# Optimization experiments

Measured on AMD Instinct MI355X. Metric: run time of the kernel, lower is better.

Reference implementation:

```python
import jax, jax.numpy as jnp
import numpy as np

N_NODES = 50000
N_EDGES = 600000
N_GRAPHS = 64
D = 128  # node/edge/global feature dim
NUM_CLASSES = 10
NUM_PASSES = 3


def setup_inputs() -> dict:
    key = jax.random.key(0)
    ks = jax.random.split(key, 12)
    node_attr = jax.random.normal(ks[0], (N_NODES, D), jnp.float32)
    edge_attr = jax.random.normal(ks[1], (N_EDGES, D), jnp.float32)
    u = jax.random.normal(ks[2], (N_GRAPHS, D), jnp.float32)
    edge_index = jax.random.randint(ks[3], (2, N_EDGES), 0, N_NODES, jnp.int64 if jax.config.jax_enable_x64 else jnp.int32)
    batch = jnp.sort(jax.random.randint(ks[4], (N_NODES,), 0, N_GRAPHS, jnp.int32))
    s = 1.0 / np.sqrt(D)
    We_w = jax.random.normal(ks[5], (4 * D, D), jnp.float32) * s
    We_b = jnp.zeros((D,), jnp.float32)
    Wn_w = jax.random.normal(ks[6], (3 * D, D), jnp.float32) * s
    Wn_b = jnp.zeros((D,), jnp.float32)
    Wg_w = jax.random.normal(ks[7], (3 * D, D), jnp.float32) * s
    Wg_b = jnp.zeros((D,), jnp.float32)
    lin_w = jax.random.normal(ks[8], (3 * D, NUM_CLASSES), jnp.float32) * s
    lin_b = jnp.zeros((NUM_CLASSES,), jnp.float32)
    return {"node_attr": node_attr, "edge_attr": edge_attr, "u": u,
            "edge_index": edge_index, "batch": batch,
            "We_w": We_w, "We_b": We_b, "Wn_w": Wn_w, "Wn_b": Wn_b,
            "Wg_w": Wg_w, "Wg_b": Wg_b, "lin_w": lin_w, "lin_b": lin_b}


def _segment_mean(x, seg, num_segments):
    s = jax.ops.segment_sum(x, seg, num_segments=num_segments)
    cnt = jax.ops.segment_sum(jnp.ones((x.shape[0],), x.dtype), seg, num_segments=num_segments)
    return s / jnp.maximum(cnt, 1.0)[:, None]


def reference(node_attr, edge_attr, u, edge_index, batch,
              We_w, We_b, Wn_w, Wn_b, Wg_w, Wg_b, lin_w, lin_b):
    src = edge_index[0]
    dst = edge_index[1]
    n_nodes = node_attr.shape[0]
    n_graphs = u.shape[0]
    edge_bar = None
    for _ in range(NUM_PASSES):
        # edge update: phi_e([h_src, h_dst, e, u[batch_src]])
        e_in = jnp.concatenate(
            [node_attr[src], node_attr[dst], edge_attr, u[batch[src]]], axis=1)
        edge_attr = jax.nn.relu(e_in @ We_w + We_b)
        # node update: mean of incoming edges per dest node, then phi_n
        edge_bar = _segment_mean(edge_attr, dst, n_nodes)  # [N, D]
        n_in = jnp.concatenate([node_attr, edge_bar, u[batch]], axis=1)
        node_attr = jax.nn.relu(n_in @ Wn_w + Wn_b)
        # global update: per-graph means, then phi_g
        node_mean = _segment_mean(node_attr, batch, n_graphs)
        eb_mean = _segment_mean(edge_bar, batch, n_graphs)
        g_in = jnp.concatenate([node_mean, eb_mean, u], axis=1)
        u = jax.nn.relu(g_in @ Wg_w + Wg_b)
    # readout: concat + global mean pool + linear classifier
    graph_attr = jnp.concatenate([node_attr, edge_bar, u[batch]], axis=1)  # [N, 3D]
    pooled = _segment_mean(graph_attr, batch, n_graphs)  # [G, 3D]
    return pooled @ lin_w + lin_b
```

## Files before the change

kernel.cpp:

```cpp
#include <hip/hip_runtime.h>
#include <math.h>

#define D 128

typedef short bf16x8 __attribute__((ext_vector_type(8)));
typedef float f32x4 __attribute__((ext_vector_type(4)));

__device__ __forceinline__ ushort f2b(float f) {
    union { float f; unsigned u; } v; v.f = f;
    unsigned r = v.u + 0x7FFFu + ((v.u >> 16) & 1u);
    return (ushort)(r >> 16);
}
__device__ __forceinline__ float b2f(ushort b) {
    union { unsigned u; float f; } v; v.u = ((unsigned)b) << 16;
    return v.f;
}
__device__ __forceinline__ void gl_lds16(const void* g, void* l) {
    __builtin_amdgcn_global_load_lds(
        (const __attribute__((address_space(1))) void*)g,
        (__attribute__((address_space(3))) void*)l, 16, 0, 0);
}
__device__ __forceinline__ int lower_bound_i(const int* __restrict__ a, int n, int v) {
    int lo = 0, hi = n;
    while (lo < hi) { int m = (lo + hi) >> 1; if (a[m] < v) lo = m + 1; else hi = m; }
    return lo;
}

__global__ void count_kernel(const int* __restrict__ dst, int* __restrict__ cnt, int E) {
    int e = blockIdx.x * blockDim.x + threadIdx.x;
    if (e < E) atomicAdd(&cnt[dst[e]], 1);
}

__global__ void scan_kernel(const int* __restrict__ cnt, int* __restrict__ offs, int N) {
    __shared__ int part[1024];
    const int t = threadIdx.x;
    const int chunk = (N + 1023) >> 10;
    int lo = t * chunk; if (lo > N) lo = N;
    int hi = lo + chunk; if (hi > N) hi = N;
    int s = 0;
    for (int i = lo; i < hi; ++i) s += cnt[i];
    part[t] = s;
    __syncthreads();
    if (t == 0) {
        int a = 0;
        for (int i = 0; i < 1024; ++i) { int v = part[i]; part[i] = a; a += v; }
        offs[N] = a;
    }
    __syncthreads();
    int a = part[t];
    for (int i = lo; i < hi; ++i) { offs[i] = a; a += cnt[i]; }
}

__global__ void scatter_kernel(const int* __restrict__ dst, const int* __restrict__ offs,
                               int* __restrict__ fill, int* __restrict__ csr, int E) {
    int e = blockIdx.x * blockDim.x + threadIdx.x;
    if (e < E) {
        int d = dst[e];
        int p = offs[d] + atomicAdd(&fill[d], 1);
        csr[p] = e;
    }
}

__global__ void f2b_kernel(const float* __restrict__ in, ushort* __restrict__ out, int n) {
    int i = blockIdx.x * blockDim.x + threadIdx.x;
    if (i < n) out[i] = f2b(in[i]);
}

__global__ void conv_edge_kernel(float* __restrict__ edge, int E) {
    int gid = blockIdx.x * blockDim.x + threadIdx.x;
    if (gid < E * 32) {
        int row = gid >> 5, q = gid & 31;
        float4 v = *(const float4*)(edge + (size_t)row * D + q * 4);
        ushort4 o;
        o.x = f2b(v.x); o.y = f2b(v.y); o.z = f2b(v.z); o.w = f2b(v.w);
        *(ushort4*)((ushort*)edge + (size_t)row * 256 + q * 4) = o;
    }
}

__global__ void transpose_w(const float* __restrict__ W, ushort* __restrict__ Wt, int K) {
    int i = blockIdx.x * blockDim.x + threadIdx.x;
    if (i < K * D) { int k = i >> 7, n = i & 127; Wt[(size_t)n * K + k] = f2b(W[i]); }
}

__global__ __launch_bounds__(256) void edge_gemm(
    const ushort* __restrict__ node_bf, ushort* __restrict__ edge_u,
    const ushort* __restrict__ u_bf,
    const int* __restrict__ src, const int* __restrict__ dst,
    const int* __restrict__ batch,
    const ushort* __restrict__ Wt, const float* __restrict__ bias, int E)
{
    __shared__ ushort As[128 * 32];
    __shared__ ushort Bs[128 * 32];
    __shared__ int rs[128], rd[128], rb[128];

    const int tid = threadIdx.x;
    const int w = tid >> 6, l = tid & 63;
    const int e0 = blockIdx.x * 128;

    if (tid < 128) {
        int e = e0 + tid; if (e >= E) e = E - 1;
        int s = src[e];
        rs[tid] = s; rd[tid] = dst[e]; rb[tid] = batch[s];
    }

    f32x4 acc[4][4];
#pragma unroll
    for (int i = 0; i < 4; ++i)
#pragma unroll
        for (int j = 0; j < 4; ++j) acc[i][j] = (f32x4)0.0f;

    const int wm = (w >> 1) * 64, wn = (w & 1) * 64;
    float bj4[4];
#pragma unroll
    for (int j = 0; j < 4; ++j) bj4[j] = bias[wn + j * 16 + (l & 15)];

    const int srow = l >> 2;
    const int part = (l & 3) * 8;

    __syncthreads();

    for (int c = 0; c < 16; ++c) {
        const int srcsel = c >> 2;
        const int kl = (c & 3) * 32;

#pragma unroll
        for (int t = 0; t < 2; ++t) {
            const int s = w + t * 4;
            const int row = s * 16 + srow;
            const ushort* gp;
            if (srcsel == 0)      gp = node_bf + (size_t)rs[row] * D + kl + part;
            else if (srcsel == 1) gp = node_bf + (size_t)rd[row] * D + kl + part;
            else if (srcsel == 2) { int e = e0 + row; if (e >= E) e = E - 1;
                                    gp = edge_u + (size_t)e * 256 + kl + part; }
            else                  gp = u_bf + (size_t)rb[row] * D + kl + part;
            gl_lds16(gp, &As[s * 512]);
        }
#pragma unroll
        for (int t = 0; t < 2; ++t) {
            const int s = w + t * 4;
            const int n = s * 16 + srow;
            gl_lds16(Wt + (size_t)n * 512 + c * 32 + part, &Bs[s * 512]);
        }
        __syncthreads();

        bf16x8 af[4], bfr[4];
#pragma unroll
        for (int i = 0; i < 4; ++i)
            af[i] = *(const bf16x8*)&As[(wm + i * 16 + (l & 15)) * 32 + (l >> 4) * 8];
#pragma unroll
        for (int j = 0; j < 4; ++j)
            bfr[j] = *(const bf16x8*)&Bs[(wn + j * 16 + (l & 15)) * 32 + (l >> 4) * 8];
#pragma unroll
        for (int i = 0; i < 4; ++i)
#pragma unroll
            for (int j = 0; j < 4; ++j)
                acc[i][j] = __builtin_amdgcn_mfma_f32_16x16x32_bf16(af[i], bfr[j], acc[i][j], 0, 0, 0);
        __syncthreads();
    }

#pragma unroll
    for (int i = 0; i < 4; ++i) {
#pragma unroll
        for (int r = 0; r < 4; ++r) {
            const int m = wm + i * 16 + (l >> 4) * 4 + r;
            const int e = e0 + m;
            if (e < E) {
                ushort* ep = edge_u + (size_t)e * 256;
#pragma unroll
                for (int j = 0; j < 4; ++j) {
                    float v = fmaxf(acc[i][j][r] + bj4[j], 0.0f);
                    ep[wn + j * 16 + (l & 15)] = f2b(v);
                }
            }
        }
    }
}

__global__ void gather_ebar(const ushort* __restrict__ edge_u, const int* __restrict__ offs,
                            const int* __restrict__ csr, ushort* __restrict__ ebar_bf, int N)
{
    int n = blockIdx.x * 2 + (threadIdx.x >> 7);
    int col = threadIdx.x & 127;
    if (n >= N) return;
    int lo = offs[n], hi = offs[n + 1];
    float s = 0.0f;
    for (int j = lo; j < hi; ++j) {
        int e = csr[j];
        s += b2f(edge_u[(size_t)e * 256 + col]);
    }
    ebar_bf[(size_t)n * D + col] = f2b(s / (float)max(hi - lo, 1));
}

__global__ __launch_bounds__(256) void node_gemm(
    ushort* __restrict__ node_bf, const ushort* __restrict__ ebar_bf,
    const ushort* __restrict__ u_bf, const int* __restrict__ batch,
    const ushort* __restrict__ Wt, const float* __restrict__ bias, int N)
{
    __shared__ ushort As[128 * 32];
    __shared__ ushort Bs[128 * 32];
    __shared__ int rb[128];

    const int tid = threadIdx.x;
    const int w = tid >> 6, l = tid & 63;
    const int n0 = blockIdx.x * 128;

    if (tid < 128) {
        int n = n0 + tid; if (n >= N) n = N - 1;
        rb[tid] = batch[n];
    }

    f32x4 acc[4][4];
#pragma unroll
    for (int i = 0; i < 4; ++i)
#pragma unroll
        for (int j = 0; j < 4; ++j) acc[i][j] = (f32x4)0.0f;

    const int wm = (w >> 1) * 64, wn = (w & 1) * 64;
    float bj4[4];
#pragma unroll
    for (int j = 0; j < 4; ++j) bj4[j] = bias[wn + j * 16 + (l & 15)];

    const int srow = l >> 2;
    const int part = (l & 3) * 8;

    __syncthreads();

    for (int c = 0; c < 12; ++c) {
        const int srcsel = c >> 2;
        const int kl = (c & 3) * 32;

#pragma unroll
        for (int t = 0; t < 2; ++t) {
            const int s = w + t * 4;
            const int row = s * 16 + srow;
            int n = n0 + row; if (n >= N) n = N - 1;
            const ushort* gp;
            if (srcsel == 0)      gp = node_bf + (size_t)n * D + kl + part;
            else if (srcsel == 1) gp = ebar_bf + (size_t)n * D + kl + part;
            else                  gp = u_bf + (size_t)rb[row] * D + kl + part;
            gl_lds16(gp, &As[s * 512]);
        }
#pragma unroll
        for (int t = 0; t < 2; ++t) {
            const int s = w + t * 4;
            const int n = s * 16 + srow;
            gl_lds16(Wt + (size_t)n * 384 + c * 32 + part, &Bs[s * 512]);
        }
        __syncthreads();

        bf16x8 af[4], bfr[4];
#pragma unroll
        for (int i = 0; i < 4; ++i)
            af[i] = *(const bf16x8*)&As[(wm + i * 16 + (l & 15)) * 32 + (l >> 4) * 8];
#pragma unroll
        for (int j = 0; j < 4; ++j)
            bfr[j] = *(const bf16x8*)&Bs[(wn + j * 16 + (l & 15)) * 32 + (l >> 4) * 8];
#pragma unroll
        for (int i = 0; i < 4; ++i)
#pragma unroll
            for (int j = 0; j < 4; ++j)
                acc[i][j] = __builtin_amdgcn_mfma_f32_16x16x32_bf16(af[i], bfr[j], acc[i][j], 0, 0, 0);
        __syncthreads();
    }

#pragma unroll
    for (int i = 0; i < 4; ++i) {
#pragma unroll
        for (int r = 0; r < 4; ++r) {
            const int m = wm + i * 16 + (l >> 4) * 4 + r;
            const int n = n0 + m;
            if (n < N) {
#pragma unroll
                for (int j = 0; j < 4; ++j) {
                    float v = fmaxf(acc[i][j][r] + bj4[j], 0.0f);
                    node_bf[(size_t)n * D + wn + j * 16 + (l & 15)] = f2b(v);
                }
            }
        }
    }
}

__global__ void reduce_partial(
    const ushort* __restrict__ node_bf, const ushort* __restrict__ ebar_bf,
    const int* __restrict__ batch,
    float* __restrict__ nsum, float* __restrict__ esum, int N)
{
    const int col = threadIdx.x & 127;
    const int half = threadIdx.x >> 7;
    const int r0 = blockIdx.x * 128;
    float sn = 0.0f, se = 0.0f;
    int cur = -1;
    for (int ri = half; ri < 128; ri += 2) {
        int r = r0 + ri;
        if (r >= N) break;
        int g = batch[r];
        if (g != cur) {
            if (cur >= 0) {
                atomicAdd(&nsum[cur * D + col], sn);
                atomicAdd(&esum[cur * D + col], se);
            }
            cur = g; sn = 0.0f; se = 0.0f;
        }
        sn += b2f(node_bf[(size_t)r * D + col]);
        se += b2f(ebar_bf[(size_t)r * D + col]);
    }
    if (cur >= 0) {
        atomicAdd(&nsum[cur * D + col], sn);
        atomicAdd(&esum[cur * D + col], se);
    }
}

__global__ void finalize_means(
    const float* __restrict__ nsum, const float* __restrict__ esum,
    const int* __restrict__ batch,
    float* __restrict__ nmean, float* __restrict__ emean, int N)
{
    const int g = blockIdx.x;
    const int j = threadIdx.x;
    __shared__ int cnt_s;
    if (j == 0) {
        int lo = lower_bound_i(batch, N, g);
        int hi = lower_bound_i(batch, N, g + 1);
        cnt_s = hi - lo;
    }
    __syncthreads();
    float inv = 1.0f / (float)max(cnt_s, 1);
    nmean[g * D + j] = nsum[g * D + j] * inv;
    emean[g * D + j] = esum[g * D + j] * inv;
}

__global__ void global_kernel(
    const float* __restrict__ nmean, const float* __restrict__ emean,
    float* __restrict__ u, ushort* __restrict__ u_bf,
    const float* __restrict__ W, const float* __restrict__ bias)
{
    __shared__ float gin[384];
    const int g = blockIdx.x;
    const int j = threadIdx.x;
    gin[j]       = nmean[g * D + j];
    gin[128 + j] = emean[g * D + j];
    gin[256 + j] = u[g * D + j];
    __syncthreads();
    float s = bias[j];
    for (int k = 0; k < 384; ++k) s += gin[k] * W[(size_t)k * D + j];
    float v = fmaxf(s, 0.0f);
    u[g * D + j] = v;
    u_bf[g * D + j] = f2b(v);
}

__global__ void out_kernel(
    const float* __restrict__ nmean, const float* __restrict__ emean,
    const float* __restrict__ u, const int* __restrict__ batch,
    const float* __restrict__ lw, const float* __restrict__ lb,
    float* __restrict__ out, int N, int NC)
{
    __shared__ float pin[384];
    __shared__ int cntg;
    const int g = blockIdx.x;
    const int t = threadIdx.x;
    if (t == 0) {
        int lo = lower_bound_i(batch, N, g);
        int hi = lower_bound_i(batch, N, g + 1);
        cntg = hi - lo;
    }
    __syncthreads();
    if (t < 128)       pin[t] = nmean[g * D + t];
    else if (t < 256)  pin[t] = emean[g * D + (t - 128)];
    else               pin[t] = (cntg > 0) ? u[g * D + (t - 256)] : 0.0f;
    __syncthreads();
    int c = t >> 5, wv = t & 31;
    if (c < NC) {
        float s = 0.0f;
        for (int k = wv; k < 384; k += 32) s += pin[k] * lw[(size_t)k * NC + c];
#pragma unroll
        for (int off = 16; off > 0; off >>= 1) s += __shfl_down(s, off, 32);
        if (wv == 0) out[g * NC + c] = s + lb[c];
    }
}

extern "C" void kernel_launch(void* const* d_in, const int* in_sizes, int n_in,
                              void* d_out, int out_size, void* d_ws, size_t ws_size,
                              hipStream_t stream) {
    float* node = (float*)d_in[0];
    float* edge = (float*)d_in[1];
    float* u    = (float*)d_in[2];
    const int* eidx  = (const int*)d_in[3];
    const int* batch = (const int*)d_in[4];
    const float* We_w = (const float*)d_in[5];
    const float* We_b = (const float*)d_in[6];
    const float* Wn_w = (const float*)d_in[7];
    const float* Wn_b = (const float*)d_in[8];
    const float* Wg_w = (const float*)d_in[9];
    const float* Wg_b = (const float*)d_in[10];
    const float* lin_w = (const float*)d_in[11];
    const float* lin_b = (const float*)d_in[12];

    const int N = in_sizes[0] / D;
    const int E = in_sizes[3] / 2;
    const int G = in_sizes[2] / D;
    const int NC = out_size / G;
    const int* src = eidx;
    const int* dst = eidx + E;

    char* p = (char*)d_ws;
    auto carve = [&](size_t bytes) { void* r = p; p += (bytes + 255) & ~(size_t)255; return r; };
    ushort* node_bf = (ushort*)carve((size_t)N * D * 2);
    ushort* ebar_bf = (ushort*)carve((size_t)N * D * 2);
    ushort* u_bf    = (ushort*)carve((size_t)G * D * 2);
    ushort* Wet     = (ushort*)carve((size_t)512 * D * 2);
    ushort* Wnt     = (ushort*)carve((size_t)384 * D * 2);
    int*    cnt     = (int*)carve((size_t)N * 4);
    int*    offs    = (int*)carve((size_t)(N + 1) * 4);
    int*    fill    = (int*)carve((size_t)N * 4);
    int*    csr     = (int*)carve((size_t)E * 4);
    float*  nmean   = (float*)carve((size_t)G * D * 4);
    float*  emean   = (float*)carve((size_t)G * D * 4);
    float*  nsum    = (float*)carve((size_t)G * D * 4);
    float*  esum    = (float*)carve((size_t)G * D * 4);

    ushort* edge_u = (ushort*)edge;

    hipMemsetAsync(cnt, 0, (size_t)N * 4, stream);
    hipMemsetAsync(fill, 0, (size_t)N * 4, stream);
    count_kernel<<<(E + 255) / 256, 256, 0, stream>>>(dst, cnt, E);
    scan_kernel<<<1, 1024, 0, stream>>>(cnt, offs, N);
    scatter_kernel<<<(E + 255) / 256, 256, 0, stream>>>(dst, offs, fill, csr, E);

    f2b_kernel<<<(N * D + 255) / 256, 256, 0, stream>>>(node, node_bf, N * D);
    f2b_kernel<<<(G * D + 255) / 256, 256, 0, stream>>>(u, u_bf, G * D);
    transpose_w<<<(512 * D + 255) / 256, 256, 0, stream>>>(We_w, Wet, 512);
    transpose_w<<<(384 * D + 255) / 256, 256, 0, stream>>>(Wn_w, Wnt, 384);
    conv_edge_kernel<<<(E * 32 + 255) / 256, 256, 0, stream>>>(edge, E);

    const int edge_blocks = (E + 127) / 128;
    const int node_blocks = (N + 127) / 128;
    const int red_blocks  = (N + 127) / 128;

    for (int pass = 0; pass < 3; ++pass) {
        edge_gemm<<<edge_blocks, 256, 0, stream>>>(node_bf, edge_u, u_bf, src, dst, batch,
                                                   Wet, We_b, E);
        gather_ebar<<<(N + 1) / 2, 256, 0, stream>>>(edge_u, offs, csr, ebar_bf, N);
        node_gemm<<<node_blocks, 256, 0, stream>>>(node_bf, ebar_bf, u_bf, batch,
                                                   Wnt, Wn_b, N);
        hipMemsetAsync(nsum, 0, (size_t)G * D * 4, stream);
        hipMemsetAsync(esum, 0, (size_t)G * D * 4, stream);
        reduce_partial<<<red_blocks, 256, 0, stream>>>(node_bf, ebar_bf, batch, nsum, esum, N);
        finalize_means<<<G, 128, 0, stream>>>(nsum, esum, batch, nmean, emean, N);
        global_kernel<<<G, 128, 0, stream>>>(nmean, emean, u, u_bf, Wg_w, Wg_b);
    }
    out_kernel<<<G, 384, 0, stream>>>(nmean, emean, u, batch, lin_w, lin_b,
                                      (float*)d_out, N, NC);
}
```

Before: 1.505 ms.

## Fuse prep kernels, enlarge edge GEMM tile, vectorize gather, merge global update

The five conversion and transpose kernels become one prep kernel, and finalize_means is merged with global_kernel. The merged kernel zeroes the sums itself, so the per-pass memsets go away and the setup memsets become one. The edge GEMM tile grows to 256 rows by the full 128 columns per block, with each wave doing 64x128. This halves the weight loads per row and the block count, but doubles accumulator registers (launch bounds 256,2). gather_ebar now uses 32 threads per node with ushort4 loads to cut per-edge load instructions, trading the fewer launches and less traffic against higher register pressure and possibly lower occupancy in the edge GEMM.

Measured after the change: 1.240 ms. 1.21x faster.

```diff
diff --git a/kernel.cpp b/kernel.cpp
--- a/kernel.cpp
+++ b/kernel.cpp
@@ -61,58 +61,77 @@
     }
 }
 
-__global__ void f2b_kernel(const float* __restrict__ in, ushort* __restrict__ out, int n) {
-    int i = blockIdx.x * blockDim.x + threadIdx.x;
-    if (i < n) out[i] = f2b(in[i]);
-}
-
-__global__ void conv_edge_kernel(float* __restrict__ edge, int E) {
-    int gid = blockIdx.x * blockDim.x + threadIdx.x;
-    if (gid < E * 32) {
+__global__ void prep_kernel(
+    float* __restrict__ edge,
+    const float* __restrict__ node, ushort* __restrict__ node_bf,
+    const float* __restrict__ u, ushort* __restrict__ u_bf,
+    const float* __restrict__ We_w, ushort* __restrict__ Wet,
+    const float* __restrict__ Wn_w, ushort* __restrict__ Wnt,
+    int N, int G, int E)
+{
+    const int gid = blockIdx.x * 256 + threadIdx.x;
+    const int c0 = E * 32;
+    const int c1 = c0 + N * D / 4;
+    const int c2 = c1 + G * D / 4;
+    const int c3 = c2 + 512 * D;
+    const int c4 = c3 + 384 * D;
+    if (gid < c0) {
         int row = gid >> 5, q = gid & 31;
         float4 v = *(const float4*)(edge + (size_t)row * D + q * 4);
-        ushort4 o;
-        o.x = f2b(v.x); o.y = f2b(v.y); o.z = f2b(v.z); o.w = f2b(v.w);
+        ushort4 o; o.x = f2b(v.x); o.y = f2b(v.y); o.z = f2b(v.z); o.w = f2b(v.w);
         *(ushort4*)((ushort*)edge + (size_t)row * 256 + q * 4) = o;
-    }
-}
-
-__global__ void transpose_w(const float* __restrict__ W, ushort* __restrict__ Wt, int K) {
-    int i = blockIdx.x * blockDim.x + threadIdx.x;
-    if (i < K * D) { int k = i >> 7, n = i & 127; Wt[(size_t)n * K + k] = f2b(W[i]); }
-}
-
-__global__ __launch_bounds__(256) void edge_gemm(
+    } else if (gid < c1) {
+        int i = (gid - c0) * 4;
+        float4 v = *(const float4*)(node + i);
+        ushort4 o; o.x = f2b(v.x); o.y = f2b(v.y); o.z = f2b(v.z); o.w = f2b(v.w);
+        *(ushort4*)(node_bf + i) = o;
+    } else if (gid < c2) {
+        int i = (gid - c1) * 4;
+        float4 v = *(const float4*)(u + i);
+        ushort4 o; o.x = f2b(v.x); o.y = f2b(v.y); o.z = f2b(v.z); o.w = f2b(v.w);
+        *(ushort4*)(u_bf + i) = o;
+    } else if (gid < c3) {
+        int i = gid - c2;
+        int k = i >> 7, n = i & 127;
+        Wet[(size_t)n * 512 + k] = f2b(We_w[i]);
+    } else if (gid < c4) {
+        int i = gid - c3;
+        int k = i >> 7, n = i & 127;
+        Wnt[(size_t)n * 384 + k] = f2b(Wn_w[i]);
+    }
+}
+
+__global__ __launch_bounds__(256, 2) void edge_gemm(
     const ushort* __restrict__ node_bf, ushort* __restrict__ edge_u,
     const ushort* __restrict__ u_bf,
     const int* __restrict__ src, const int* __restrict__ dst,
     const int* __restrict__ batch,
     const ushort* __restrict__ Wt, const float* __restrict__ bias, int E)
 {
-    __shared__ ushort As[128 * 32];
+    __shared__ ushort As[256 * 32];
     __shared__ ushort Bs[128 * 32];
-    __shared__ int rs[128], rd[128], rb[128];
+    __shared__ int rs[256], rd[256], rb[256];
 
     const int tid = threadIdx.x;
     const int w = tid >> 6, l = tid & 63;
-    const int e0 = blockIdx.x * 128;
-
-    if (tid < 128) {
+    const int e0 = blockIdx.x * 256;
+
+    {
         int e = e0 + tid; if (e >= E) e = E - 1;
         int s = src[e];
         rs[tid] = s; rd[tid] = dst[e]; rb[tid] = batch[s];
     }
 
-    f32x4 acc[4][4];
+    f32x4 acc[4][8];
 #pragma unroll
     for (int i = 0; i < 4; ++i)
 #pragma unroll
-        for (int j = 0; j < 4; ++j) acc[i][j] = (f32x4)0.0f;
-
-    const int wm = (w >> 1) * 64, wn = (w & 1) * 64;
-    float bj4[4];
-#pragma unroll
-    for (int j = 0; j < 4; ++j) bj4[j] = bias[wn + j * 16 + (l & 15)];
+        for (int j = 0; j < 8; ++j) acc[i][j] = (f32x4)0.0f;
+
+    const int wm = w * 64;
+    float bj8[8];
+#pragma unroll
+    for (int j = 0; j < 8; ++j) bj8[j] = bias[j * 16 + (l & 15)];
 
     const int srow = l >> 2;
     const int part = (l & 3) * 8;
@@ -124,8 +143,8 @@
         const int kl = (c & 3) * 32;
 
 #pragma unroll
-        for (int t = 0; t < 2; ++t) {
-            const int s = w + t * 4;
+        for (int t = 0; t < 4; ++t) {
+            const int s = w * 4 + t;
             const int row = s * 16 + srow;
             const ushort* gp;
             if (srcsel == 0)      gp = node_bf + (size_t)rs[row] * D + kl + part;
@@ -143,17 +162,17 @@
         }
         __syncthreads();
 
-        bf16x8 af[4], bfr[4];
+        bf16x8 af[4], bfr[8];
 #pragma unroll
         for (int i = 0; i < 4; ++i)
             af[i] = *(const bf16x8*)&As[(wm + i * 16 + (l & 15)) * 32 + (l >> 4) * 8];
 #pragma unroll
-        for (int j = 0; j < 4; ++j)
-            bfr[j] = *(const bf16x8*)&Bs[(wn + j * 16 + (l & 15)) * 32 + (l >> 4) * 8];
+        for (int j = 0; j < 8; ++j)
+            bfr[j] = *(const bf16x8*)&Bs[(j * 16 + (l & 15)) * 32 + (l >> 4) * 8];
 #pragma unroll
         for (int i = 0; i < 4; ++i)
 #pragma unroll
-            for (int j = 0; j < 4; ++j)
+            for (int j = 0; j < 8; ++j)
                 acc[i][j] = __builtin_amdgcn_mfma_f32_16x16x32_bf16(af[i], bfr[j], acc[i][j], 0, 0, 0);
         __syncthreads();
     }
@@ -167,9 +186,9 @@
             if (e < E) {
                 ushort* ep = edge_u + (size_t)e * 256;
 #pragma unroll
-                for (int j = 0; j < 4; ++j) {
-                    float v = fmaxf(acc[i][j][r] + bj4[j], 0.0f);
-                    ep[wn + j * 16 + (l & 15)] = f2b(v);
+                for (int j = 0; j < 8; ++j) {
+                    float v = fmaxf(acc[i][j][r] + bj8[j], 0.0f);
+                    ep[j * 16 + (l & 15)] = f2b(v);
                 }
             }
         }
@@ -179,16 +198,19 @@
 __global__ void gather_ebar(const ushort* __restrict__ edge_u, const int* __restrict__ offs,
                             const int* __restrict__ csr, ushort* __restrict__ ebar_bf, int N)
 {
-    int n = blockIdx.x * 2 + (threadIdx.x >> 7);
-    int col = threadIdx.x & 127;
+    int n = blockIdx.x * 8 + (threadIdx.x >> 5);
+    int q = threadIdx.x & 31;
     if (n >= N) return;
     int lo = offs[n], hi = offs[n + 1];
-    float s = 0.0f;
+    float s0 = 0.0f, s1 = 0.0f, s2 = 0.0f, s3 = 0.0f;
     for (int j = lo; j < hi; ++j) {
         int e = csr[j];
-        s += b2f(edge_u[(size_t)e * 256 + col]);
-    }
-    ebar_bf[(size_t)n * D + col] = f2b(s / (float)max(hi - lo, 1));
+        ushort4 v = *(const ushort4*)(edge_u + (size_t)e * 256 + q * 4);
+        s0 += b2f(v.x); s1 += b2f(v.y); s2 += b2f(v.z); s3 += b2f(v.w);
+    }
+    float inv = 1.0f / (float)max(hi - lo, 1);
+    ushort4 o; o.x = f2b(s0 * inv); o.y = f2b(s1 * inv); o.z = f2b(s2 * inv); o.w = f2b(s3 * inv);
+    *(ushort4*)(ebar_bf + (size_t)n * D + q * 4) = o;
 }
 
 __global__ __launch_bounds__(256) void node_gemm(
@@ -310,14 +332,17 @@
     }
 }
 
-__global__ void finalize_means(
-    const float* __restrict__ nsum, const float* __restrict__ esum,
+__global__ void finalize_global(
+    float* __restrict__ nsum, float* __restrict__ esum,
     const int* __restrict__ batch,
-    float* __restrict__ nmean, float* __restrict__ emean, int N)
-{
+    float* __restrict__ nmean, float* __restrict__ emean,
+    float* __restrict__ u, ushort* __restrict__ u_bf,
+    const float* __restrict__ W, const float* __restrict__ bias, int N)
+{
+    __shared__ float gin[384];
+    __shared__ int cnt_s;
     const int g = blockIdx.x;
     const int j = threadIdx.x;
-    __shared__ int cnt_s;
     if (j == 0) {
         int lo = lower_bound_i(batch, N, g);
         int hi = lower_bound_i(batch, N, g + 1);
@@ -325,21 +350,13 @@
     }
     __syncthreads();
     float inv = 1.0f / (float)max(cnt_s, 1);
-    nmean[g * D + j] = nsum[g * D + j] * inv;
-    emean[g * D + j] = esum[g * D + j] * inv;
-}
-
-__global__ void global_kernel(
-    const float* __restrict__ nmean, const float* __restrict__ emean,
-    float* __restrict__ u, ushort* __restrict__ u_bf,
-    const float* __restrict__ W, const float* __restrict__ bias)
-{
-    __shared__ float gin[384];
-    const int g = blockIdx.x;
-    const int j = threadIdx.x;
-    gin[j]       = nmean[g * D + j];
-    gin[128 + j] = emean[g * D + j];
-    gin[256 + j] = u[g * D + j];
+    float nm = nsum[g * D + j] * inv;
+    float em = esum[g * D + j] * inv;
+    nmean[g * D + j] = nm;
+    emean[g * D + j] = em;
+    nsum[g * D + j] = 0.0f;
+    esum[g * D + j] = 0.0f;
+    gin[j] = nm; gin[128 + j] = em; gin[256 + j] = u[g * D + j];
     __syncthreads();
     float s = bias[j];
     for (int k = 0; k < 384; ++k) s += gin[k] * W[(size_t)k * D + j];
@@ -404,49 +421,46 @@
 
     char* p = (char*)d_ws;
     auto carve = [&](size_t bytes) { void* r = p; p += (bytes + 255) & ~(size_t)255; return r; };
+    int*    cnt     = (int*)carve((size_t)N * 4);
+    int*    fill    = (int*)carve((size_t)N * 4);
+    float*  nsum    = (float*)carve((size_t)G * D * 4);
+    float*  esum    = (float*)carve((size_t)G * D * 4);
+    size_t  zspan   = (size_t)(p - (char*)cnt);
+    int*    offs    = (int*)carve((size_t)(N + 1) * 4);
+    int*    csr     = (int*)carve((size_t)E * 4);
     ushort* node_bf = (ushort*)carve((size_t)N * D * 2);
     ushort* ebar_bf = (ushort*)carve((size_t)N * D * 2);
     ushort* u_bf    = (ushort*)carve((size_t)G * D * 2);
     ushort* Wet     = (ushort*)carve((size_t)512 * D * 2);
     ushort* Wnt     = (ushort*)carve((size_t)384 * D * 2);
-    int*    cnt     = (int*)carve((size_t)N * 4);
-    int*    offs    = (int*)carve((size_t)(N + 1) * 4);
-    int*    fill    = (int*)carve((size_t)N * 4);
-    int*    csr     = (int*)carve((size_t)E * 4);
     float*  nmean   = (float*)carve((size_t)G * D * 4);
     float*  emean   = (float*)carve((size_t)G * D * 4);
-    float*  nsum    = (float*)carve((size_t)G * D * 4);
-    float*  esum    = (float*)carve((size_t)G * D * 4);
 
     ushort* edge_u = (ushort*)edge;
 
-    hipMemsetAsync(cnt, 0, (size_t)N * 4, stream);
-    hipMemsetAsync(fill, 0, (size_t)N * 4, stream);
+    hipMemsetAsync(cnt, 0, zspan, stream);
+
     count_kernel<<<(E + 255) / 256, 256, 0, stream>>>(dst, cnt, E);
     scan_kernel<<<1, 1024, 0, stream>>>(cnt, offs, N);
     scatter_kernel<<<(E + 255) / 256, 256, 0, stream>>>(dst, offs, fill, csr, E);
 
-    f2b_kernel<<<(N * D + 255) / 256, 256, 0, stream>>>(node, node_bf, N * D);
-    f2b_kernel<<<(G * D + 255) / 256, 256, 0, stream>>>(u, u_bf, G * D);
-    transpose_w<<<(512 * D + 255) / 256, 256, 0, stream>>>(We_w, Wet, 512);
-    transpose_w<<<(384 * D + 255) / 256, 256, 0, stream>>>(Wn_w, Wnt, 384);
-    conv_edge_kernel<<<(E * 32 + 255) / 256, 256, 0, stream>>>(edge, E);
-
-    const int edge_blocks = (E + 127) / 128;
+    const int prep_units = E * 32 + N * D / 4 + G * D / 4 + 512 * D + 384 * D;
+    prep_kernel<<<(prep_units + 255) / 256, 256, 0, stream>>>(
+        edge, node, node_bf, u, u_bf, We_w, Wet, Wn_w, Wnt, N, G, E);
+
+    const int edge_blocks = (E + 255) / 256;
     const int node_blocks = (N + 127) / 128;
     const int red_blocks  = (N + 127) / 128;
 
     for (int pass = 0; pass < 3; ++pass) {
         edge_gemm<<<edge_blocks, 256, 0, stream>>>(node_bf, edge_u, u_bf, src, dst, batch,
                                                    Wet, We_b, E);
-        gather_ebar<<<(N + 1) / 2, 256, 0, stream>>>(edge_u, offs, csr, ebar_bf, N);
+        gather_ebar<<<(N + 7) / 8, 256, 0, stream>>>(edge_u, offs, csr, ebar_bf, N);
         node_gemm<<<node_blocks, 256, 0, stream>>>(node_bf, ebar_bf, u_bf, batch,
                                                    Wnt, Wn_b, N);
-        hipMemsetAsync(nsum, 0, (size_t)G * D * 4, stream);
-        hipMemsetAsync(esum, 0, (size_t)G * D * 4, stream);
         reduce_partial<<<red_blocks, 256, 0, stream>>>(node_bf, ebar_bf, batch, nsum, esum, N);
-        finalize_means<<<G, 128, 0, stream>>>(nsum, esum, batch, nmean, emean, N);
-        global_kernel<<<G, 128, 0, stream>>>(nmean, emean, u, u_bf, Wg_w, Wg_b);
+        finalize_global<<<G, 128, 0, stream>>>(nsum, esum, batch, nmean, emean,
+                                               u, u_bf, Wg_w, Wg_b, N);
     }
     out_kernel<<<G, 384, 0, stream>>>(nmean, emean, u, batch, lin_w, lin_b,
                                       (float*)d_out, N, NC);
```
